# Performance work log

Hardware: AMD Instinct MI355X
Metric: run time of the kernel (lower is better)

Reference implementation:

```python
import jax, jax.numpy as jnp
import numpy as np

TEMPERATURE = 0.5  # NT-Xent temperature (SimCLR default in SACLR)
NEG_INF = -1e9


def ntxent(zi, zj, temperature=TEMPERATURE):
    """SimCLR NT-Xent between two views zi, zj of shape [B, D]."""
    B = zi.shape[0]
    z = jnp.concatenate([zi, zj], axis=0)                      # [2B, D]
    z = z / (jnp.linalg.norm(z, axis=1, keepdims=True) + 1e-8)  # cosine sim
    sim = (z @ z.T) / temperature                              # [2B, 2B]
    n = 2 * B
    sim = jnp.where(jnp.eye(n, dtype=bool), NEG_INF, sim)      # mask self
    labels = jnp.concatenate([jnp.arange(B) + B, jnp.arange(B)])
    logp = jax.nn.log_softmax(sim, axis=1)
    return -jnp.mean(logp[jnp.arange(n), labels])


def setup_inputs() -> dict:
    key = jax.random.key(0)
    k1, k2, k3 = jax.random.split(key, 3)
    B, D, W, H, CA = 512, 256, 14, 14, 8
    return {
        "global_feature": jax.random.normal(k1, (B, D), dtype=jnp.float32),
        "att": jax.random.uniform(k2, (B, CA, W, H), dtype=jnp.float32),
        "outputs": jax.random.normal(k3, (B, D, W, H), dtype=jnp.float32),
    }


def reference(global_feature, att, outputs):
    # attention = sum over attention-map channel, shape [B, W, H]
    attention = jnp.sum(att, axis=1)
    B, D, W, H = outputs.shape
    P = W * H
    # Flatten spatial positions in the same (i over W, j over H) row-major order
    # as the original nested python loops.
    local_feats = jnp.transpose(outputs, (2, 3, 0, 1)).reshape(P, B, D)   # [P, B, D]
    local_atts = jnp.transpose(attention, (1, 2, 0)).reshape(P, B)        # [P, B]

    # Faithful quirk of the original: global_feature is re-softmaxed at every
    # spatial position (it is reassigned inside the loop), so carry it in a scan.
    def step(g, xs):
        lf, la = xs
        g = jax.nn.softmax(g, axis=1)          # repeated softmax on global
        lf = jax.nn.softmax(lf, axis=1)        # softmax on local feature
        l = ntxent(lf, g) * jnp.mean(la) / P   # weighted NT-Xent term
        return g, l

    _, losses = jax.lax.scan(step, global_feature, (local_feats, local_atts))
    return jnp.sum(losses)
```

## Files before the change

kernel.cpp:

```cpp
#include <hip/hip_runtime.h>

#define B_   512
#define D_   256
#define P_   196
#define N2B  1024

#define CSCALE 1.69864364f
#define LN2    0.69314718f

typedef __attribute__((ext_vector_type(8))) short short8;
typedef __attribute__((ext_vector_type(4))) float f32x4;
typedef unsigned int u32;

#define LDSP(x) ((__attribute__((address_space(3))) u32*)(x))
#define GLBP(x) ((const __attribute__((address_space(1))) u32*)(x))

__device__ unsigned short g_Z[(size_t)P_ * N2B * D_];
__device__ float g_rowps[(size_t)P_ * 8 * N2B];
__device__ float g_pp2[P_ * 4];
__device__ float g_mApart[128 * P_];
__device__ float g_partials[P_];

static __device__ const unsigned char TROW36[36] = {
  0,0,0,0,0,0,0,0, 1,1,1,1,1,1,1, 2,2,2,2,2,2, 3,3,3,3,3, 4,4,4,4, 5,5,5, 6,6, 7};
static __device__ const unsigned char TCOL36[36] = {
  0,1,2,3,4,5,6,7, 1,2,3,4,5,6,7, 2,3,4,5,6,7, 3,4,5,6,7, 4,5,6,7, 5,6,7, 6,7, 7};

static __device__ inline unsigned short f2bf(float f) {
    union { float f; unsigned int u; } v; v.f = f;
    unsigned int u = v.u;
    return (unsigned short)((u + 0x7fffu + ((u >> 16) & 1u)) >> 16);
}
static __device__ inline float bf2f(unsigned short h) {
    union { unsigned int u; float f; } v; v.u = ((unsigned int)h) << 16;
    return v.f;
}
static __device__ inline float wave_sum(float v) {
    for (int off = 32; off > 0; off >>= 1) v += __shfl_xor(v, off, 64);
    return v;
}

__global__ __launch_bounds__(1024) void prep_kernel(const float* __restrict__ gf,
                                                    const float* __restrict__ att,
                                                    const float* __restrict__ outs) {
    __shared__ unsigned short vt[256 * 202];
    __shared__ float ss[256];
    int blk = blockIdx.x, t = threadIdx.x;

    if (blk < 32) {
        int wv = t >> 6, lane = t & 63;
        int b = blk * 16 + wv;
        float4 g = ((const float4*)(gf + (size_t)b * D_))[lane];
        for (int p = 0; p < P_; ++p) {
            float e0 = __expf(g.x), e1 = __expf(g.y), e2 = __expf(g.z), e3 = __expf(g.w);
            float s1 = e0 + e1 + e2 + e3;
            float s2 = e0 * e0 + e1 * e1 + e2 * e2 + e3 * e3;
#pragma unroll
            for (int off = 32; off > 0; off >>= 1) {
                s1 += __shfl_xor(s1, off, 64);
                s2 += __shfl_xor(s2, off, 64);
            }
            float isq = rsqrtf(s2) * CSCALE;
            ushort4 o;
            o.x = f2bf(e0 * isq); o.y = f2bf(e1 * isq); o.z = f2bf(e2 * isq); o.w = f2bf(e3 * isq);
            ((ushort4*)(g_Z + ((size_t)p * N2B + B_ + b) * D_))[lane] = o;
            float inv = 1.0f / s1;
            g.x = e0 * inv; g.y = e1 * inv; g.z = e2 * inv; g.w = e3 * inv;
        }
    } else if (blk < 64) {
        int bk = blk - 32;
        int sl = t >> 8, p = t & 255;
        if (p < P_) {
            float acc = 0.0f;
            const float* base = att + ((size_t)bk * 128 + sl * 32) * P_ + p;
            for (int r = 0; r < 32; ++r) acc += base[(size_t)r * P_];
            g_mApart[(bk * 4 + sl) * P_ + p] = acc;
        }
    } else {
        int b = blk - 64;
        const float4* src4 = (const float4*)(outs + (size_t)b * (D_ * P_));
        for (int idx = t; idx < 12544; idx += 1024) {
            int d = idx / 49, c = idx - d * 49;
            float4 v = src4[idx];
            unsigned short* dst = vt + d * 202 + c * 4;
            ushort2 a, bb;
            a.x = f2bf(v.x); a.y = f2bf(v.y); bb.x = f2bf(v.z); bb.y = f2bf(v.w);
            *(ushort2*)dst = a; *(ushort2*)(dst + 2) = bb;
        }
        __syncthreads();
        {
            int p = t >> 2; if (p > 195) p = 195;
            int s = t & 3;
            float r = 0.0f;
            for (int dd = 0; dd < 64; ++dd) {
                float v = bf2f(vt[(s * 64 + dd) * 202 + p]);
                r += __expf(2.0f * v);
            }
            r += __shfl_xor(r, 1, 64);
            r += __shfl_xor(r, 2, 64);
            if (s == 0) ss[p] = rsqrtf(r) * CSCALE;
        }
        __syncthreads();
        {
            int d = t & 255, q = t >> 8;
            for (int pi = 0; pi < 49; ++pi) {
                int p = q * 49 + pi;
                float v = bf2f(vt[d * 202 + p]);
                g_Z[((size_t)p * N2B + b) * D_ + d] = f2bf(__expf(v) * ss[p]);
            }
        }
    }
}

template<int MODE>
static __device__ inline void do_epi(const f32x4 acc[4][4], float psum[4][4], float pcs[4],
                                     float& pp, int wdiag, int lr, int r4) {
#pragma unroll
    for (int i = 0; i < 4; ++i) {
#pragma unroll
        for (int j = 0; j < 4; ++j) {
#pragma unroll
            for (int r = 0; r < 4; ++r) {
                float a = acc[i][j][r];
                float e = exp2f(a);
                if (MODE == 1) {
                    if (wdiag && i == j) e = (r4 + r == lr) ? 0.0f : e;
                }
                psum[i][r] += e;
                if (MODE != 1) pcs[j] += e;
                if (MODE == 2) {
                    if (wdiag && i == j && (r4 + r == lr)) pp += a * LN2;
                }
            }
        }
    }
}

__global__ __launch_bounds__(256, 4) void sim_kernel() {
    __shared__ __align__(16) unsigned short As[128 * 64];
    __shared__ __align__(16) unsigned short Bs[128 * 64];
    __shared__ float combuf[512];
    __shared__ float ppred[4];

    int lin0 = blockIdx.x;
    int xcd = lin0 & 7, slot = lin0 >> 3;
    int lin = xcd * 882 + slot;
    int p = lin / 36;
    int t36 = lin - p * 36;
    int trow = TROW36[t36], tcol = TCOL36[t36];

    int tid = threadIdx.x;
    int wv = tid >> 6, lane = tid & 63;
    int wr = wv >> 1, wc = wv & 1;
    int lr = lane & 15;
    int lk16 = (lane >> 4) * 16;

    const char* zb = (const char*)g_Z + (size_t)p * ((size_t)N2B * D_ * 2);
    const char* gA = zb + (size_t)trow * (128 * 512);
    const char* gB = zb + (size_t)tcol * (128 * 512);
    int lsub = (lane >> 3) * 512 + (((lane & 7) ^ (lane >> 3)) << 4);

    f32x4 acc[4][4];
#pragma unroll
    for (int i = 0; i < 4; ++i)
#pragma unroll
        for (int j = 0; j < 4; ++j)
            acc[i][j] = (f32x4){0.0f, 0.0f, 0.0f, 0.0f};

    for (int ko = 0; ko < 4; ++ko) {
#pragma unroll
        for (int it = 0; it < 4; ++it) {
            int s = it * 4 + wv;
            int go = s * 4096 + ko * 128 + lsub;
            __builtin_amdgcn_global_load_lds(GLBP(gA + go), LDSP((char*)As + s * 1024), 16, 0, 0);
            __builtin_amdgcn_global_load_lds(GLBP(gB + go), LDSP((char*)Bs + s * 1024), 16, 0, 0);
        }
        __syncthreads();
#pragma unroll
        for (int ks = 0; ks < 2; ++ks) {
            int kswz = (ks * 64 + lk16) ^ ((lr & 7) << 4);
            short8 a[4], b[4];
#pragma unroll
            for (int i = 0; i < 4; ++i) {
                a[i] = *(const short8*)((const char*)As + (wr * 64 + i * 16 + lr) * 128 + kswz);
                b[i] = *(const short8*)((const char*)Bs + (wc * 64 + i * 16 + lr) * 128 + kswz);
            }
#pragma unroll
            for (int i = 0; i < 4; ++i)
#pragma unroll
                for (int j = 0; j < 4; ++j)
                    acc[i][j] = __builtin_amdgcn_mfma_f32_16x16x32_bf16(a[i], b[j], acc[i][j], 0, 0, 0);
        }
        __syncthreads();
    }

    bool DIAG = (trow == tcol);
    bool PART = (trow < 4) && (tcol == trow + 4);
    int wdiag = (wr == wc);
    int r4 = (lane >> 4) * 4;
    float psum[4][4];
    float pcs[4] = {0.0f, 0.0f, 0.0f, 0.0f};
    float pp = 0.0f;
#pragma unroll
    for (int i = 0; i < 4; ++i)
#pragma unroll
        for (int r = 0; r < 4; ++r) psum[i][r] = 0.0f;

    if (DIAG)      do_epi<1>(acc, psum, pcs, pp, wdiag, lr, r4);
    else if (PART) do_epi<2>(acc, psum, pcs, pp, wdiag, lr, r4);
    else           do_epi<0>(acc, psum, pcs, pp, wdiag, lr, r4);

    float* rowbuf = combuf;
    float* colbuf = combuf + 256;
#pragma unroll
    for (int i = 0; i < 4; ++i)
#pragma unroll
        for (int r = 0; r < 4; ++r) {
            float ps = psum[i][r];
            ps += __shfl_xor(ps, 1, 64);
            ps += __shfl_xor(ps, 2, 64);
            ps += __shfl_xor(ps, 4, 64);
            ps += __shfl_xor(ps, 8, 64);
            if (lr == 0) rowbuf[wc * 128 + wr * 64 + i * 16 + r4 + r] = ps;
        }
    if (!DIAG) {
#pragma unroll
        for (int j = 0; j < 4; ++j) {
            float pc = pcs[j];
            pc += __shfl_xor(pc, 16, 64);
            pc += __shfl_xor(pc, 32, 64);
            if (lane < 16) colbuf[wr * 128 + wc * 64 + j * 16 + lane] = pc;
        }
    }
    if (PART) {
        float pw = wave_sum(pp);
        if (lane == 0) ppred[wv] = pw;
    }
    __syncthreads();

    if (tid < 128) {
        float v = rowbuf[tid] + rowbuf[128 + tid];
        g_rowps[((size_t)p * 8 + tcol) * N2B + trow * 128 + tid] = v;
    } else if (!DIAG) {
        int x = tid - 128;
        float v = colbuf[x] + colbuf[128 + x];
        g_rowps[((size_t)p * 8 + trow) * N2B + tcol * 128 + x] = v;
    }
    if (PART && tid == 0)
        g_pp2[p * 4 + trow] = 2.0f * (ppred[0] + ppred[1] + ppred[2] + ppred[3]);
}

__global__ __launch_bounds__(256) void rowreduce_kernel() {
    int p = blockIdx.x, t = threadIdx.x;
    const float* base = g_rowps + (size_t)p * 8 * N2B;
    float s = 0.0f;
    for (int r = t; r < N2B; r += 256) {
        float S = 0.0f;
#pragma unroll
        for (int k = 0; k < 8; ++k) S += base[(size_t)k * N2B + r];
        s += __logf(S);
    }
    s = wave_sum(s);
    __shared__ float red[4];
    int wv = t >> 6, lane = t & 63;
    if (lane == 0) red[wv] = s;
    __syncthreads();
    if (t == 0) {
        float tot = red[0] + red[1] + red[2] + red[3];
        float pp = g_pp2[p * 4 + 0] + g_pp2[p * 4 + 1] + g_pp2[p * 4 + 2] + g_pp2[p * 4 + 3];
        float ma = 0.0f;
        for (int k = 0; k < 128; ++k) ma += g_mApart[k * P_ + p];
        g_partials[p] = (tot - pp) * (ma * (1.0f / B_));
    }
}

__global__ __launch_bounds__(256) void final_kernel(float* __restrict__ out) {
    int t = threadIdx.x;
    float s = (t < P_) ? g_partials[t] : 0.0f;
    s = wave_sum(s);
    __shared__ float red[4];
    int wv = t >> 6, lane = t & 63;
    if (lane == 0) red[wv] = s;
    __syncthreads();
    if (t == 0) out[0] = (red[0] + red[1] + red[2] + red[3]) * (1.0f / ((float)N2B * (float)P_));
}

extern "C" void kernel_launch(void* const* d_in, const int* in_sizes, int n_in,
                              void* d_out, int out_size, void* d_ws, size_t ws_size,
                              hipStream_t stream) {
    const float* gf   = (const float*)d_in[0];
    const float* att  = (const float*)d_in[1];
    const float* outs = (const float*)d_in[2];
    float* out = (float*)d_out;

    hipLaunchKernelGGL(prep_kernel, dim3(576), dim3(1024), 0, stream, gf, att, outs);
    hipLaunchKernelGGL(sim_kernel, dim3(P_ * 36), dim3(256), 0, stream);
    hipLaunchKernelGGL(rowreduce_kernel, dim3(P_), dim3(256), 0, stream);
    hipLaunchKernelGGL(final_kernel, dim3(1), dim3(256), 0, stream, out);
}
```

Before: 323.9 us.

## Split prep into two finer-grained kernels and exploit symmetry in diagonal sim tiles

The single large-block prep kernel becomes two launches with 256-thread blocks. The first computes per-position sum-of-squares partials over D quarters using shared atomics. The second builds the normalized bf16 Z rows over D halves, which raises parallelism and occupancy. In diagonal tiles of the similarity kernel, the B operand load is dropped because A equals B, and one wave skips its redundant lower-triangle block, obtaining its row sums from another wave's column sums. This adds a launch, re-reads the outputs tensor twice, and adds LDS atomic contention.

```diff
diff --git a/kernel.cpp b/kernel.cpp
--- a/kernel.cpp
+++ b/kernel.cpp
@@ -7,6 +7,7 @@
 
 #define CSCALE 1.69864364f
 #define LN2    0.69314718f
+#define T2L    2.8853900817779268f
 
 typedef __attribute__((ext_vector_type(8))) short short8;
 typedef __attribute__((ext_vector_type(4))) float f32x4;
@@ -19,6 +20,7 @@
 __device__ float g_rowps[(size_t)P_ * 8 * N2B];
 __device__ float g_pp2[P_ * 4];
 __device__ float g_mApart[128 * P_];
+__device__ float g_dpart[(size_t)B_ * 4 * P_];
 __device__ float g_partials[P_];
 
 static __device__ const unsigned char TROW36[36] = {
@@ -40,16 +42,15 @@
     return v;
 }
 
-__global__ __launch_bounds__(1024) void prep_kernel(const float* __restrict__ gf,
+__global__ __launch_bounds__(256) void prep1_kernel(const float* __restrict__ gf,
                                                     const float* __restrict__ att,
                                                     const float* __restrict__ outs) {
-    __shared__ unsigned short vt[256 * 202];
-    __shared__ float ss[256];
+    __shared__ float ssw[4][200];
     int blk = blockIdx.x, t = threadIdx.x;
 
-    if (blk < 32) {
+    if (blk < 128) {
         int wv = t >> 6, lane = t & 63;
-        int b = blk * 16 + wv;
+        int b = blk * 4 + wv;
         float4 g = ((const float4*)(gf + (size_t)b * D_))[lane];
         for (int p = 0; p < P_; ++p) {
             float e0 = __expf(g.x), e1 = __expf(g.y), e2 = __expf(g.z), e3 = __expf(g.w);
@@ -67,48 +68,65 @@
             float inv = 1.0f / s1;
             g.x = e0 * inv; g.y = e1 * inv; g.z = e2 * inv; g.w = e3 * inv;
         }
-    } else if (blk < 64) {
-        int bk = blk - 32;
-        int sl = t >> 8, p = t & 255;
-        if (p < P_) {
+    } else if (blk < 256) {
+        int bk = blk - 128;
+        if (t < P_) {
             float acc = 0.0f;
-            const float* base = att + ((size_t)bk * 128 + sl * 32) * P_ + p;
+            const float* base = att + (size_t)bk * 32 * P_ + t;
             for (int r = 0; r < 32; ++r) acc += base[(size_t)r * P_];
-            g_mApart[(bk * 4 + sl) * P_ + p] = acc;
+            g_mApart[bk * P_ + t] = acc;
         }
     } else {
-        int b = blk - 64;
-        const float4* src4 = (const float4*)(outs + (size_t)b * (D_ * P_));
-        for (int idx = t; idx < 12544; idx += 1024) {
-            int d = idx / 49, c = idx - d * 49;
+        int id = blk - 256;
+        int b = id >> 2, dq = id & 3;
+        int wv = t >> 6;
+        for (int i = t; i < 800; i += 256) ((float*)ssw)[i] = 0.0f;
+        __syncthreads();
+        const float4* src4 = (const float4*)(outs + (size_t)b * (D_ * P_) + dq * (64 * P_));
+        for (int idx = t; idx < 3136; idx += 256) {
             float4 v = src4[idx];
-            unsigned short* dst = vt + d * 202 + c * 4;
-            ushort2 a, bb;
-            a.x = f2bf(v.x); a.y = f2bf(v.y); bb.x = f2bf(v.z); bb.y = f2bf(v.w);
-            *(ushort2*)dst = a; *(ushort2*)(dst + 2) = bb;
+            int c4 = (idx % 49) * 4;
+            atomicAdd(&ssw[wv][c4 + 0], exp2f(v.x * T2L));
+            atomicAdd(&ssw[wv][c4 + 1], exp2f(v.y * T2L));
+            atomicAdd(&ssw[wv][c4 + 2], exp2f(v.z * T2L));
+            atomicAdd(&ssw[wv][c4 + 3], exp2f(v.w * T2L));
         }
         __syncthreads();
-        {
-            int p = t >> 2; if (p > 195) p = 195;
-            int s = t & 3;
-            float r = 0.0f;
-            for (int dd = 0; dd < 64; ++dd) {
-                float v = bf2f(vt[(s * 64 + dd) * 202 + p]);
-                r += __expf(2.0f * v);
-            }
-            r += __shfl_xor(r, 1, 64);
-            r += __shfl_xor(r, 2, 64);
-            if (s == 0) ss[p] = rsqrtf(r) * CSCALE;
-        }
-        __syncthreads();
-        {
-            int d = t & 255, q = t >> 8;
-            for (int pi = 0; pi < 49; ++pi) {
-                int p = q * 49 + pi;
-                float v = bf2f(vt[d * 202 + p]);
-                g_Z[((size_t)p * N2B + b) * D_ + d] = f2bf(__expf(v) * ss[p]);
-            }
-        }
+        if (t < P_)
+            g_dpart[(size_t)id * P_ + t] = ssw[0][t] + ssw[1][t] + ssw[2][t] + ssw[3][t];
+    }
+}
+
+__global__ __launch_bounds__(256) void prep2_kernel(const float* __restrict__ outs) {
+    __shared__ unsigned short vt[128 * 202];
+    __shared__ float ss[P_];
+    int blk = blockIdx.x, t = threadIdx.x;
+    int b = blk >> 1, dh = blk & 1;
+    const float4* src4 = (const float4*)(outs + (size_t)b * (D_ * P_) + dh * (128 * P_));
+    for (int idx = t; idx < 6272; idx += 256) {
+        int d = idx / 49, c = idx - d * 49;
+        float4 v = src4[idx];
+        unsigned short* dst = vt + d * 202 + c * 4;
+        ushort2 a, bb;
+        a.x = f2bf(v.x); a.y = f2bf(v.y); bb.x = f2bf(v.z); bb.y = f2bf(v.w);
+        *(ushort2*)dst = a; *(ushort2*)(dst + 2) = bb;
+    }
+    if (t < P_) {
+        const float* dp = g_dpart + (size_t)(b * 4) * P_ + t;
+        float s = dp[0] + dp[P_] + dp[2 * P_] + dp[3 * P_];
+        ss[t] = rsqrtf(s) * CSCALE;
+    }
+    __syncthreads();
+    int w = t >> 6, l = t & 63;
+    for (int i = 0; i < 49; ++i) {
+        int p = w * 49 + i;
+        float v0 = bf2f(vt[(2 * l) * 202 + p]);
+        float v1 = bf2f(vt[(2 * l + 1) * 202 + p]);
+        float sc = ss[p];
+        ushort2 o;
+        o.x = f2bf(__expf(v0) * sc);
+        o.y = f2bf(__expf(v1) * sc);
+        *(ushort2*)(g_Z + ((size_t)p * N2B + b) * D_ + dh * 128 + 2 * l) = o;
     }
 }
 
@@ -127,7 +145,7 @@
                     if (wdiag && i == j) e = (r4 + r == lr) ? 0.0f : e;
                 }
                 psum[i][r] += e;
-                if (MODE != 1) pcs[j] += e;
+                pcs[j] += e;
                 if (MODE == 2) {
                     if (wdiag && i == j && (r4 + r == lr)) pp += a * LN2;
                 }
@@ -148,12 +166,15 @@
     int p = lin / 36;
     int t36 = lin - p * 36;
     int trow = TROW36[t36], tcol = TCOL36[t36];
+    bool DIAG = (trow == tcol);
+    bool PART = (trow < 4) && (tcol == trow + 4);
 
     int tid = threadIdx.x;
     int wv = tid >> 6, lane = tid & 63;
     int wr = wv >> 1, wc = wv & 1;
     int lr = lane & 15;
     int lk16 = (lane >> 4) * 16;
+    bool skipw = DIAG && (wv == 2);
 
     const char* zb = (const char*)g_Z + (size_t)p * ((size_t)N2B * D_ * 2);
     const char* gA = zb + (size_t)trow * (128 * 512);
@@ -167,35 +188,38 @@
         for (int j = 0; j < 4; ++j)
             acc[i][j] = (f32x4){0.0f, 0.0f, 0.0f, 0.0f};
 
+    const char* BsR = DIAG ? (const char*)As : (const char*)Bs;
+
     for (int ko = 0; ko < 4; ++ko) {
 #pragma unroll
         for (int it = 0; it < 4; ++it) {
             int s = it * 4 + wv;
             int go = s * 4096 + ko * 128 + lsub;
             __builtin_amdgcn_global_load_lds(GLBP(gA + go), LDSP((char*)As + s * 1024), 16, 0, 0);
-            __builtin_amdgcn_global_load_lds(GLBP(gB + go), LDSP((char*)Bs + s * 1024), 16, 0, 0);
+            if (!DIAG)
+                __builtin_amdgcn_global_load_lds(GLBP(gB + go), LDSP((char*)Bs + s * 1024), 16, 0, 0);
         }
         __syncthreads();
-#pragma unroll
-        for (int ks = 0; ks < 2; ++ks) {
-            int kswz = (ks * 64 + lk16) ^ ((lr & 7) << 4);
-            short8 a[4], b[4];
-#pragma unroll
-            for (int i = 0; i < 4; ++i) {
-                a[i] = *(const short8*)((const char*)As + (wr * 64 + i * 16 + lr) * 128 + kswz);
-                b[i] = *(const short8*)((const char*)Bs + (wc * 64 + i * 16 + lr) * 128 + kswz);
+        if (!skipw) {
+#pragma unroll
+            for (int ks = 0; ks < 2; ++ks) {
+                int kswz = (ks * 64 + lk16) ^ ((lr & 7) << 4);
+                short8 a[4], b[4];
+#pragma unroll
+                for (int i = 0; i < 4; ++i) {
+                    a[i] = *(const short8*)((const char*)As + (wr * 64 + i * 16 + lr) * 128 + kswz);
+                    b[i] = *(const short8*)(BsR + (wc * 64 + i * 16 + lr) * 128 + kswz);
+                }
+#pragma unroll
+                for (int i = 0; i < 4; ++i)
+#pragma unroll
+                    for (int j = 0; j < 4; ++j)
+                        acc[i][j] = __builtin_amdgcn_mfma_f32_16x16x32_bf16(a[i], b[j], acc[i][j], 0, 0, 0);
             }
-#pragma unroll
-            for (int i = 0; i < 4; ++i)
-#pragma unroll
-                for (int j = 0; j < 4; ++j)
-                    acc[i][j] = __builtin_amdgcn_mfma_f32_16x16x32_bf16(a[i], b[j], acc[i][j], 0, 0, 0);
         }
         __syncthreads();
     }
 
-    bool DIAG = (trow == tcol);
-    bool PART = (trow < 4) && (tcol == trow + 4);
     int wdiag = (wr == wc);
     int r4 = (lane >> 4) * 4;
     float psum[4][4];
@@ -206,23 +230,27 @@
 #pragma unroll
         for (int r = 0; r < 4; ++r) psum[i][r] = 0.0f;
 
-    if (DIAG)      do_epi<1>(acc, psum, pcs, pp, wdiag, lr, r4);
-    else if (PART) do_epi<2>(acc, psum, pcs, pp, wdiag, lr, r4);
-    else           do_epi<0>(acc, psum, pcs, pp, wdiag, lr, r4);
+    if (!skipw) {
+        if (DIAG)      do_epi<1>(acc, psum, pcs, pp, wdiag, lr, r4);
+        else if (PART) do_epi<2>(acc, psum, pcs, pp, wdiag, lr, r4);
+        else           do_epi<0>(acc, psum, pcs, pp, wdiag, lr, r4);
+    }
 
     float* rowbuf = combuf;
     float* colbuf = combuf + 256;
-#pragma unroll
-    for (int i = 0; i < 4; ++i)
-#pragma unroll
-        for (int r = 0; r < 4; ++r) {
-            float ps = psum[i][r];
-            ps += __shfl_xor(ps, 1, 64);
-            ps += __shfl_xor(ps, 2, 64);
-            ps += __shfl_xor(ps, 4, 64);
-            ps += __shfl_xor(ps, 8, 64);
-            if (lr == 0) rowbuf[wc * 128 + wr * 64 + i * 16 + r4 + r] = ps;
-        }
+    if (!skipw) {
+#pragma unroll
+        for (int i = 0; i < 4; ++i)
+#pragma unroll
+            for (int r = 0; r < 4; ++r) {
+                float ps = psum[i][r];
+                ps += __shfl_xor(ps, 1, 64);
+                ps += __shfl_xor(ps, 2, 64);
+                ps += __shfl_xor(ps, 4, 64);
+                ps += __shfl_xor(ps, 8, 64);
+                if (lr == 0) rowbuf[wc * 128 + wr * 64 + i * 16 + r4 + r] = ps;
+            }
+    }
     if (!DIAG) {
 #pragma unroll
         for (int j = 0; j < 4; ++j) {
@@ -230,6 +258,14 @@
             pc += __shfl_xor(pc, 16, 64);
             pc += __shfl_xor(pc, 32, 64);
             if (lane < 16) colbuf[wr * 128 + wc * 64 + j * 16 + lane] = pc;
+        }
+    } else if (wv == 1) {
+#pragma unroll
+        for (int j = 0; j < 4; ++j) {
+            float pc = pcs[j];
+            pc += __shfl_xor(pc, 16, 64);
+            pc += __shfl_xor(pc, 32, 64);
+            if (lane < 16) rowbuf[64 + j * 16 + lane] = pc;
         }
     }
     if (PART) {
@@ -293,7 +329,8 @@
     const float* outs = (const float*)d_in[2];
     float* out = (float*)d_out;
 
-    hipLaunchKernelGGL(prep_kernel, dim3(576), dim3(1024), 0, stream, gf, att, outs);
+    hipLaunchKernelGGL(prep1_kernel, dim3(2304), dim3(256), 0, stream, gf, att, outs);
+    hipLaunchKernelGGL(prep2_kernel, dim3(B_ * 2), dim3(256), 0, stream, outs);
     hipLaunchKernelGGL(sim_kernel, dim3(P_ * 36), dim3(256), 0, stream);
     hipLaunchKernelGGL(rowreduce_kernel, dim3(P_), dim3(256), 0, stream);
     hipLaunchKernelGGL(final_kernel, dim3(1), dim3(256), 0, stream, out);
```

Measured after the change: 454.5 us. +40.3%, slower.
